# Kernel tuning notes

Hardware: AMD Instinct MI355X
Metric: run time of the kernel (lower is better)

Reference implementation:

```python
import jax, jax.numpy as jnp
import numpy as np

B, C, H, W = 32, 256, 7, 7
HEADS = 8
DIM_HEAD = 64
INNER = HEADS * DIM_HEAD  # 512
N_ANGLES = 16
KS = 5
GROUPS = 32
EPS = 1e-5


def setup_inputs() -> dict:
    key = jax.random.key(0)
    ks = jax.random.split(key, 16)
    w = lambda k, shp: jax.random.normal(k, shp, jnp.float32) * 0.05
    return {
        'x': jax.random.normal(ks[0], (B, C, H, W), jnp.float32),
        'gn_g': jnp.ones((C,), jnp.float32), 'gn_b': jnp.zeros((C,), jnp.float32),
        'sa_w1': w(ks[1], (C // 8, C)), 'sa_b1': jnp.zeros((C // 8,), jnp.float32),
        'sa_w2': w(ks[2], (C, C // 8)), 'sa_b2': jnp.zeros((C,), jnp.float32),
        'sa_gn_g': jnp.ones((C,), jnp.float32), 'sa_gn_b': jnp.zeros((C,), jnp.float32),
        'ra_gn_g': jnp.ones((C,), jnp.float32), 'ra_gn_b': jnp.zeros((C,), jnp.float32),
        'ra_qkv_w': w(ks[3], (3 * C, C)),
        'ra_proj_w': w(ks[4], (C, C)), 'ra_proj_b': jnp.zeros((C,), jnp.float32),
        'aa_ln_g': jnp.ones((C,), jnp.float32), 'aa_ln_b': jnp.zeros((C,), jnp.float32),
        'aa_qkv_w': w(ks[5], (3 * INNER, C)),
        'aa_relpos': w(ks[6], (2 * 7 - 1, 2 * 7 - 1, HEADS)),
        'aa_out_w': w(ks[7], (C, INNER)), 'aa_out_b': jnp.zeros((C,), jnp.float32),
        'ad_dir_w': w(ks[8], (N_ANGLES, C, C, KS, KS)),
        'ad_ap_w1': w(ks[9], (128, C)), 'ad_ap_b1': jnp.zeros((128,), jnp.float32),
        'ad_ap_w2': w(ks[10], (N_ANGLES, 128)), 'ad_ap_b2': jnp.zeros((N_ANGLES,), jnp.float32),
        'ad_proj_w': w(ks[11], (C, C)), 'ad_proj_b': jnp.zeros((C,), jnp.float32),
        'gate_w': w(ks[12], (4, C)), 'gate_b': jnp.zeros((4,), jnp.float32),
        'proj_w': w(ks[13], (C, C)), 'proj_b': jnp.zeros((C,), jnp.float32),
    }


def _gn(x, g, b):
    Bx, Cx, Hx, Wx = x.shape
    xr = x.reshape(Bx, GROUPS, -1)
    m = xr.mean(-1, keepdims=True)
    v = xr.var(-1, keepdims=True)
    xn = ((xr - m) * jax.lax.rsqrt(v + EPS)).reshape(Bx, Cx, Hx, Wx)
    return xn * g[None, :, None, None] + b[None, :, None, None]


def _c1(x, w, b=None):
    y = jnp.einsum('bchw,oc->bohw', x, w)
    return y if b is None else y + b[None, :, None, None]


def _rot_attn_pass(x, qkv_w):
    Bx, Cx, Hx, Wx = x.shape
    d = Cx // HEADS
    q, k, v = jnp.split(_c1(x, qkv_w), 3, axis=1)
    sh = lambda t: t.reshape(Bx, HEADS, d, Hx * Wx).transpose(0, 1, 3, 2)  # b h n d
    q, k, v = sh(q), sh(k), sh(v)
    a = jax.nn.softmax(jnp.einsum('bhid,bhjd->bhij', q, k) * (d ** -0.5), axis=-1)
    o = jnp.einsum('bhij,bhjd->bhid', a, v)
    return o.transpose(0, 1, 3, 2).reshape(Bx, Cx, Hx, Wx)


def _forward(x, gn_g, gn_b, sa_w1, sa_b1, sa_w2, sa_b2, sa_gn_g, sa_gn_b,
             ra_gn_g, ra_gn_b, ra_qkv_w, ra_proj_w, ra_proj_b,
             aa_ln_g, aa_ln_b, aa_qkv_w, aa_relpos, aa_out_w, aa_out_b,
             ad_dir_w, ad_ap_w1, ad_ap_b1, ad_ap_w2, ad_ap_b2, ad_proj_w, ad_proj_b,
             gate_w, gate_b, proj_w, proj_b):
    normed = _gn(x, gn_g, gn_b)

    # --- SpatialAttention branch ---
    wts = jax.nn.sigmoid(_c1(jax.nn.relu(_c1(normed, sa_w1, sa_b1)), sa_w2, sa_b2))
    spatial = _gn(normed * wts + normed, sa_gn_g, sa_gn_b)

    # --- RotationAwareAttention branch: 4 rot90 passes, max-fused ---
    xr = _gn(normed, ra_gn_g, ra_gn_b)
    r0 = _rot_attn_pass(xr, ra_qkv_w)
    r1 = jnp.rot90(_rot_attn_pass(jnp.rot90(xr, 1, (2, 3)), ra_qkv_w), 3, (2, 3))
    r2 = jnp.rot90(_rot_attn_pass(jnp.rot90(xr, 2, (2, 3)), ra_qkv_w), 2, (2, 3))
    r3 = jnp.rot90(_rot_attn_pass(jnp.rot90(xr, 3, (2, 3)), ra_qkv_w), 1, (2, 3))
    mx = jnp.maximum(jnp.maximum(r0, r1), jnp.maximum(r2, r3))
    rotation = _c1(mx, ra_proj_w, ra_proj_b) + normed

    # --- AngleAwareSelfAttention branch (rel-pos-biased MHSA over 49 tokens) ---
    Nn = H * W
    t = normed.reshape(B, C, Nn).transpose(0, 2, 1)  # [B,N,C]
    mu = t.mean(-1, keepdims=True)
    var = t.var(-1, keepdims=True)
    tn = (t - mu) * jax.lax.rsqrt(var + EPS) * aa_ln_g + aa_ln_b
    q, k, v = jnp.split(jnp.einsum('bnc,oc->bno', tn, aa_qkv_w), 3, axis=-1)
    sh = lambda u: u.reshape(B, Nn, HEADS, DIM_HEAD).transpose(0, 2, 1, 3)
    q, k, v = sh(q), sh(k), sh(v)
    dots = jnp.einsum('bhid,bhjd->bhij', q, k) * (DIM_HEAD ** -0.5)
    idx = jnp.arange(Nn)
    yi, xi = idx // W, idx % W
    dy = yi[None, :] - yi[:, None] + (H - 1)  # offsets into 13x13 table
    dx = xi[None, :] - xi[:, None] + (W - 1)
    bias = aa_relpos[dy, dx].transpose(2, 0, 1)[None]  # [1,heads,N,N]
    attn = jax.nn.softmax(dots + bias, axis=-1)
    o = jnp.einsum('bhij,bhjd->bhid', attn, v).transpose(0, 2, 1, 3).reshape(B, Nn, INNER)
    o = jnp.einsum('bni,oi->bno', o, aa_out_w) + aa_out_b
    angle = o.transpose(0, 2, 1).reshape(B, C, H, W) + normed

    # --- AngleAdaptiveAttention branch: 16 directional 5x5 convs + learned softmax gate ---
    dir_out = jax.lax.conv_general_dilated(
        normed, ad_dir_w.reshape(N_ANGLES * C, C, KS, KS), (1, 1), 'SAME',
        dimension_numbers=('NCHW', 'OIHW', 'NCHW')).reshape(B, N_ANGLES, C, H, W)
    gap = normed.mean((2, 3))  # [B,C]
    h1 = jax.nn.relu(gap @ ad_ap_w1.T + ad_ap_b1)
    aw = jax.nn.softmax(h1 @ ad_ap_w2.T + ad_ap_b2, axis=1)  # [B,16]
    comb = jnp.einsum('bkchw,bk->bchw', dir_out, aw)
    adaptive = _c1(comb, ad_proj_w, ad_proj_b) + normed

    # --- gated fusion ---
    gates = jax.nn.softmax(_c1(x, gate_w, gate_b), axis=1)  # [B,4,H,W]
    fused = (spatial * gates[:, 0:1] + rotation * gates[:, 1:2]
             + angle * gates[:, 2:3] + adaptive * gates[:, 3:4])
    return _c1(fused, proj_w, proj_b) + x


def reference(x, gn_g, gn_b, sa_w1, sa_b1, sa_w2, sa_b2, sa_gn_g, sa_gn_b,
              ra_gn_g, ra_gn_b, ra_qkv_w, ra_proj_w, ra_proj_b,
              aa_ln_g, aa_ln_b, aa_qkv_w, aa_relpos, aa_out_w, aa_out_b,
              ad_dir_w, ad_ap_w1, ad_ap_b1, ad_ap_w2, ad_ap_b2, ad_proj_w, ad_proj_b,
              gate_w, gate_b, proj_w, proj_b):
    return _forward(x, gn_g, gn_b, sa_w1, sa_b1, sa_w2, sa_b2, sa_gn_g, sa_gn_b,
                    ra_gn_g, ra_gn_b, ra_qkv_w, ra_proj_w, ra_proj_b,
                    aa_ln_g, aa_ln_b, aa_qkv_w, aa_relpos, aa_out_w, aa_out_b,
                    ad_dir_w, ad_ap_w1, ad_ap_b1, ad_ap_w2, ad_ap_b2, ad_proj_w, ad_proj_b,
                    gate_w, gate_b, proj_w, proj_b)
```

## Files before the change

kernel.cpp:

```cpp
#include <hip/hip_runtime.h>

#define EPS 1e-5f
typedef unsigned short u16;
typedef unsigned int u32;
typedef float f32x4 __attribute__((ext_vector_type(4)));
typedef short bf16x8 __attribute__((ext_vector_type(8)));

__device__ __forceinline__ float bf2f(u16 h){
  return __uint_as_float(((u32)h) << 16);
}
__device__ __forceinline__ u16 f2bf(float f){
  u32 u = __float_as_uint(f);
  u += 0x7fffu + ((u >> 16) & 1u);
  return (u16)(u >> 16);
}
__device__ __forceinline__ u32 pk2(float lo, float hi){
  return ((u32)f2bf(hi) << 16) | (u32)f2bf(lo);
}
union BF8 { bf16x8 v; u32 u[4]; };

__global__ __launch_bounds__(256) void k_prep1(
    const float* __restrict__ x, const float* __restrict__ gn_g, const float* __restrict__ gn_b,
    const float* __restrict__ ra_g, const float* __restrict__ ra_b,
    float* __restrict__ normed, float* __restrict__ xr, float* __restrict__ gap)
{
  int ch = blockIdx.x, b = blockIdx.y;
  int c0 = ch * 32;
  __shared__ float xs[1568], ns[1568];
  const float* xb = x + ((size_t)b * 256 + c0) * 49;
  for (int i = threadIdx.x; i < 1568; i += 256) xs[i] = xb[i];
  __syncthreads();
  int wv = threadIdx.x >> 6, lane = threadIdx.x & 63;
  const float* gsrc = xs + wv * 392;
  float* ndst = ns + wv * 392;
  float s = 0.f, ss = 0.f;
  for (int i = lane; i < 392; i += 64){ float v = gsrc[i]; s += v; ss += v * v; }
  for (int off = 32; off; off >>= 1){ s += __shfl_down(s, off); ss += __shfl_down(ss, off); }
  s = __shfl(s, 0); ss = __shfl(ss, 0);
  float m = s / 392.f, rs = rsqrtf(ss / 392.f - m * m + EPS);
  for (int i = lane; i < 392; i += 64){
    int c = c0 + wv * 8 + i / 49;
    ndst[i] = (gsrc[i] - m) * rs * gn_g[c] + gn_b[c];
  }
  __syncthreads();
  float* nb = normed + ((size_t)b * 256 + c0) * 49;
  for (int i = threadIdx.x; i < 1568; i += 256) nb[i] = ns[i];
  if (threadIdx.x < 32){
    float g2 = 0.f; const float* rp = ns + threadIdx.x * 49;
    for (int p = 0; p < 49; p++) g2 += rp[p];
    gap[(size_t)b * 256 + c0 + threadIdx.x] = g2 * (1.f / 49.f);
  }
  s = 0.f; ss = 0.f;
  for (int i = lane; i < 392; i += 64){ float v = ndst[i]; s += v; ss += v * v; }
  for (int off = 32; off; off >>= 1){ s += __shfl_down(s, off); ss += __shfl_down(ss, off); }
  s = __shfl(s, 0); ss = __shfl(ss, 0);
  m = s / 392.f; rs = rsqrtf(ss / 392.f - m * m + EPS);
  float* xrb = xr + ((size_t)b * 256 + c0) * 49;
  for (int i = lane; i < 392; i += 64){
    int c = c0 + wv * 8 + i / 49;
    xrb[wv * 392 + i] = (ndst[i] - m) * rs * ra_g[c] + ra_b[c];
  }
}

__global__ __launch_bounds__(256) void k_pos(
    const float* __restrict__ x, const float* __restrict__ normed,
    const float* __restrict__ gate_w, const float* __restrict__ gate_b,
    float* __restrict__ gates_g, float* __restrict__ lnm_g, float* __restrict__ lnr_g)
{
  int pc = blockIdx.x, b = blockIdx.y;
  __shared__ float gw[1024];
  for (int i = threadIdx.x; i < 1024; i += 256) gw[i] = gate_w[i];
  __syncthreads();
  int wv = threadIdx.x >> 6, lane = threadIdx.x & 63;
  for (int pi = wv; pi < 7; pi += 4){
    int p = pc * 7 + pi;
    const float* nb = normed + (size_t)b * 12544 + p;
    const float* xb = x + (size_t)b * 12544 + p;
    float s = 0.f, ss = 0.f, g0 = 0.f, g1 = 0.f, g2 = 0.f, g3 = 0.f;
    for (int c = lane; c < 256; c += 64){
      float nv = nb[c * 49];
      float xv = xb[c * 49];
      s += nv; ss += nv * nv;
      g0 += xv * gw[c]; g1 += xv * gw[256 + c];
      g2 += xv * gw[512 + c]; g3 += xv * gw[768 + c];
    }
    for (int off = 32; off; off >>= 1){
      s += __shfl_down(s, off); ss += __shfl_down(ss, off);
      g0 += __shfl_down(g0, off); g1 += __shfl_down(g1, off);
      g2 += __shfl_down(g2, off); g3 += __shfl_down(g3, off);
    }
    if (lane == 0){
      float mu = s / 256.f;
      lnm_g[b * 49 + p] = mu;
      lnr_g[b * 49 + p] = rsqrtf(ss / 256.f - mu * mu + EPS);
      g0 += gate_b[0]; g1 += gate_b[1]; g2 += gate_b[2]; g3 += gate_b[3];
      float mx = fmaxf(fmaxf(g0, g1), fmaxf(g2, g3));
      float e0 = __expf(g0 - mx), e1 = __expf(g1 - mx), e2 = __expf(g2 - mx), e3 = __expf(g3 - mx);
      float inv = 1.f / (e0 + e1 + e2 + e3);
      float* gg = gates_g + (size_t)b * 196 + p;
      gg[0] = e0 * inv; gg[49] = e1 * inv; gg[98] = e2 * inv; gg[147] = e3 * inv;
    }
  }
}

__global__ __launch_bounds__(256) void k_h1aw(
    const float* __restrict__ normed, const float* __restrict__ sa_w1, const float* __restrict__ sa_b1,
    const float* __restrict__ ap_w1, const float* __restrict__ ap_b1,
    const float* __restrict__ ap_w2, const float* __restrict__ ap_b2,
    const float* __restrict__ gap_g,
    float* __restrict__ h1_g, float* __restrict__ aw_g)
{
  int xb2 = blockIdx.x, b = blockIdx.y;
  int t = threadIdx.x;
  if (xb2 == 7){
    __shared__ float gaps[256], h[128], lg[16];
    gaps[t] = gap_g[b * 256 + t];
    __syncthreads();
    if (t < 128){
      float s = ap_b1[t];
      const float* wr = ap_w1 + t * 256;
      #pragma unroll 4
      for (int c = 0; c < 256; c++) s += gaps[c] * wr[c];
      h[t] = fmaxf(s, 0.f);
    }
    __syncthreads();
    if (t < 16){
      float s = ap_b2[t];
      const float* wr = ap_w2 + t * 128;
      #pragma unroll 4
      for (int o = 0; o < 128; o++) s += h[o] * wr[o];
      lg[t] = s;
    }
    __syncthreads();
    if (t == 0){
      float mx = -1e30f;
      for (int k = 0; k < 16; k++) mx = fmaxf(mx, lg[k]);
      float e[16], sm = 0.f;
      for (int k = 0; k < 16; k++){ e[k] = __expf(lg[k] - mx); sm += e[k]; }
      float inv = 1.f / sm;
      for (int k = 0; k < 16; k++) aw_g[b * 16 + k] = e[k] * inv;
    }
    return;
  }
  __shared__ float w1t[256 * 33];
  __shared__ float ns2[256 * 7];
  int p0 = xb2 * 7;
  for (int i = t; i < 8192; i += 256){
    int o = i >> 8, c = i & 255;
    w1t[c * 33 + o] = sa_w1[i];
  }
  for (int i = t; i < 1792; i += 256){
    int c = i / 7, pl = i - c * 7;
    ns2[i] = normed[(size_t)b * 12544 + c * 49 + p0 + pl];
  }
  __syncthreads();
  if (t < 224){
    int pl = t >> 5, o = t & 31;
    float s = sa_b1[o];
    #pragma unroll 8
    for (int c = 0; c < 256; c++) s += ns2[c * 7 + pl] * w1t[c * 33 + o];
    h1_g[(size_t)b * 1568 + (p0 + pl) * 32 + o] = fmaxf(s, 0.f);
  }
}

__global__ __launch_bounds__(256) void k_spatial(
    const float* __restrict__ normed, const float* __restrict__ h1_g,
    const float* __restrict__ sa_w2, const float* __restrict__ sa_b2,
    const float* __restrict__ sa_g, const float* __restrict__ sa_bb,
    float* __restrict__ spat_g)
{
  int gc = blockIdx.x, b = blockIdx.y;
  __shared__ float h1s[49 * 33];
  __shared__ float w2s[1024];
  int t = threadIdx.x;
  for (int i = t; i < 1568; i += 256){
    int p = i >> 5, o = i & 31;
    h1s[p * 33 + o] = h1_g[(size_t)b * 1568 + i];
  }
  for (int i = t; i < 1024; i += 256) w2s[i] = sa_w2[gc * 1024 + i];
  __syncthreads();
  int wv = t >> 6, lane = t & 63;
  int cg0 = wv * 8;
  const float* nb = normed + (size_t)b * 12544 + (gc * 32 + cg0) * 49;
  float tmp[7];
  float s = 0.f, ss = 0.f;
  #pragma unroll
  for (int j = 0; j < 7; j++){
    int i = lane + 64 * j;
    float v = 0.f;
    if (i < 392){
      int c = i / 49;
      const float* wr = w2s + (cg0 + c) * 32;
      const float* hp = h1s + (i - c * 49) * 33;
      float d = sa_b2[gc * 32 + cg0 + c];
      #pragma unroll
      for (int o = 0; o < 32; o++) d += hp[o] * wr[o];
      v = nb[i] * (1.f + 1.f / (1.f + __expf(-d)));
      s += v; ss += v * v;
    }
    tmp[j] = v;
  }
  for (int off = 32; off; off >>= 1){ s += __shfl_down(s, off); ss += __shfl_down(ss, off); }
  s = __shfl(s, 0); ss = __shfl(ss, 0);
  float m = s / 392.f, rs = rsqrtf(ss / 392.f - m * m + EPS);
  float* sb = spat_g + (size_t)b * 12544 + (gc * 32 + cg0) * 49;
  #pragma unroll
  for (int j = 0; j < 7; j++){
    int i = lane + 64 * j;
    if (i < 392){
      int c = gc * 32 + cg0 + i / 49;
      sb[i] = (tmp[j] - m) * rs * sa_g[c] + sa_bb[c];
    }
  }
}

__global__ __launch_bounds__(256) void k_weff(
    const float* __restrict__ W, const float* __restrict__ aw, u16* __restrict__ weff)
{
  __shared__ float aws[512];
  for (int i = threadIdx.x; i < 512; i += 256) aws[i] = aw[i];
  size_t j = (size_t)blockIdx.x * 1024 + (size_t)threadIdx.x * 4;
  float4 wv[16];
  #pragma unroll
  for (int k = 0; k < 16; k++)
    wv[k] = *(const float4*)(W + (size_t)k * 1638400 + j);
  __syncthreads();
  #pragma unroll 1
  for (int b = 0; b < 32; b++){
    const float* a = aws + b * 16;
    float a0 = 0.f, a1 = 0.f, a2 = 0.f, a3 = 0.f;
    #pragma unroll
    for (int k = 0; k < 16; k++){
      float s = a[k];
      a0 += s * wv[k].x; a1 += s * wv[k].y; a2 += s * wv[k].z; a3 += s * wv[k].w;
    }
    ushort4 o;
    o.x = f2bf(a0); o.y = f2bf(a1); o.z = f2bf(a2); o.w = f2bf(a3);
    *(ushort4*)(weff + (size_t)b * 1638400 + j) = o;
  }
}

__global__ __launch_bounds__(256) void k_conv(
    const u16* __restrict__ weff, const float* __restrict__ normed, float* __restrict__ comb_part)
{
  int part = blockIdx.x, b = blockIdx.y;
  int co = threadIdx.x;
  __shared__ float xs[784];
  const float* nb = normed + ((size_t)b * 256 + part * 16) * 49;
  for (int i = co; i < 784; i += 256) xs[i] = nb[i];
  __syncthreads();
  float acc[49];
  #pragma unroll
  for (int p = 0; p < 49; p++) acc[p] = 0.f;
  const u16* wr = weff + (size_t)b * 1638400 + (size_t)co * 6400 + part * 400;
  #pragma unroll 1
  for (int ci = 0; ci < 16; ci++){
    float ximg[49];
    #pragma unroll
    for (int p = 0; p < 49; p++) ximg[p] = xs[ci * 49 + p];
    float wv[25];
    #pragma unroll
    for (int s2 = 0; s2 < 25; s2++) wv[s2] = bf2f(wr[ci * 25 + s2]);
    #pragma unroll
    for (int sy = 0; sy < 5; sy++){
      #pragma unroll
      for (int sx = 0; sx < 5; sx++){
        float w = wv[sy * 5 + sx];
        #pragma unroll
        for (int py = 0; py < 7; py++){
          int iy = py + sy - 2;
          if (iy < 0 || iy >= 7) continue;
          #pragma unroll
          for (int px = 0; px < 7; px++){
            int ix = px + sx - 2;
            if (ix < 0 || ix >= 7) continue;
            acc[py * 7 + px] += w * ximg[iy * 7 + ix];
          }
        }
      }
    }
  }
  float* op = comb_part + (((size_t)part * 32 + b) * 256 + co) * 49;
  #pragma unroll
  for (int p = 0; p < 49; p++) op[p] = acc[p];
}

__global__ __launch_bounds__(256) void k_comb_reduce(
    const float* __restrict__ part, float* __restrict__ comb)
{
  int i = blockIdx.x * 256 + threadIdx.x;
  if (i >= 100352) return;
  float a0 = 0.f, a1 = 0.f, a2 = 0.f, a3 = 0.f;
  #pragma unroll
  for (int p = 0; p < 16; p++){
    float4 v = ((const float4*)part)[(size_t)p * 100352 + i];
    a0 += v.x; a1 += v.y; a2 += v.z; a3 += v.w;
  }
  float4 o; o.x = a0; o.y = a1; o.z = a2; o.w = a3;
  ((float4*)comb)[i] = o;
}

__device__ __forceinline__ void mfma_gemm_dev(
    const float* __restrict__ W, const float* __restrict__ bias,
    const float* __restrict__ act, const float* __restrict__ res,
    float* __restrict__ out, int M, int K, int m0blk, int p0, int b,
    const float* __restrict__ lnm, const float* __restrict__ lnr,
    const float* __restrict__ lng, const float* __restrict__ lnb)
{
  int wv = threadIdx.x >> 6, lane = threadIdx.x & 63;
  int lo = lane & 15, hi = lane >> 4;
  int m0 = m0blk + wv * 32;
  int p = p0 + lo;
  bool pok = p < 49;
  const float* ab = act + (size_t)b * K * 49;
  float lm = 0.f, lr = 0.f;
  if (lng && pok){ lm = lnm[p]; lr = lnr[p]; }
  f32x4 acc0 = {0.f, 0.f, 0.f, 0.f};
  f32x4 acc1 = {0.f, 0.f, 0.f, 0.f};
  const float* wr0 = W + (size_t)(m0 + lo) * K + hi * 8;
  const float* wr1 = W + (size_t)(m0 + 16 + lo) * K + hi * 8;
  for (int k0 = 0; k0 < K; k0 += 32){
    int kb = k0 + hi * 8;
    float4 a0lo = *(const float4*)(wr0 + k0);
    float4 a0hi = *(const float4*)(wr0 + k0 + 4);
    float4 a1lo = *(const float4*)(wr1 + k0);
    float4 a1hi = *(const float4*)(wr1 + k0 + 4);
    float bv[8];
    if (pok){
      const float* ap = ab + (size_t)kb * 49 + p;
      #pragma unroll
      for (int i = 0; i < 8; i++) bv[i] = ap[i * 49];
      if (lng){
        #pragma unroll
        for (int i = 0; i < 8; i++) bv[i] = (bv[i] - lm) * lr * lng[kb + i] + lnb[kb + i];
      }
    } else {
      #pragma unroll
      for (int i = 0; i < 8; i++) bv[i] = 0.f;
    }
    BF8 A0, A1, B;
    A0.u[0] = pk2(a0lo.x, a0lo.y); A0.u[1] = pk2(a0lo.z, a0lo.w);
    A0.u[2] = pk2(a0hi.x, a0hi.y); A0.u[3] = pk2(a0hi.z, a0hi.w);
    A1.u[0] = pk2(a1lo.x, a1lo.y); A1.u[1] = pk2(a1lo.z, a1lo.w);
    A1.u[2] = pk2(a1hi.x, a1hi.y); A1.u[3] = pk2(a1hi.z, a1hi.w);
    B.u[0] = pk2(bv[0], bv[1]); B.u[1] = pk2(bv[2], bv[3]);
    B.u[2] = pk2(bv[4], bv[5]); B.u[3] = pk2(bv[6], bv[7]);
    acc0 = __builtin_amdgcn_mfma_f32_16x16x32_bf16(A0.v, B.v, acc0, 0, 0, 0);
    acc1 = __builtin_amdgcn_mfma_f32_16x16x32_bf16(A1.v, B.v, acc1, 0, 0, 0);
  }
  if (pok){
    #pragma unroll
    for (int r = 0; r < 4; r++){
      int m = m0 + hi * 4 + r;
      size_t idx = ((size_t)b * M + m) * 49 + p;
      float v = acc0[r] + (bias ? bias[m] : 0.f);
      if (res) v += res[idx];
      out[idx] = v;
      int m2 = m + 16;
      size_t idx2 = idx + 16 * 49;
      float v2 = acc1[r] + (bias ? bias[m2] : 0.f);
      if (res) v2 += res[idx2];
      out[idx2] = v2;
    }
  }
}

__global__ __launch_bounds__(256) void k_qkv(
    const float* __restrict__ ra_w, const float* __restrict__ aa_w,
    const float* __restrict__ xr, const float* __restrict__ normed,
    const float* __restrict__ lnm, const float* __restrict__ lnr,
    const float* __restrict__ ln_g, const float* __restrict__ ln_b,
    float* __restrict__ ra_qkv, float* __restrict__ aa_qkv)
{
  int bx = blockIdx.x, b = blockIdx.y;
  if (bx < 24){
    int m0 = (bx >> 2) * 128, p0 = (bx & 3) * 16;
    mfma_gemm_dev(ra_w, nullptr, xr, nullptr, ra_qkv, 768, 256, m0, p0, b,
                  nullptr, nullptr, nullptr, nullptr);
  } else {
    int bx2 = bx - 24;
    int m0 = (bx2 >> 2) * 128, p0 = (bx2 & 3) * 16;
    mfma_gemm_dev(aa_w, nullptr, normed, nullptr, aa_qkv, 1536, 256, m0, p0, b,
                  lnm + b * 49, lnr + b * 49, ln_g, ln_b);
  }
}

__global__ __launch_bounds__(256) void k_proj3(
    const float* __restrict__ ra_pw, const float* __restrict__ ra_pb, const float* __restrict__ r0,
    const float* __restrict__ aa_ow, const float* __restrict__ aa_ob, const float* __restrict__ aa_o,
    const float* __restrict__ ad_pw, const float* __restrict__ ad_pb, const float* __restrict__ comb,
    const float* __restrict__ normed,
    float* __restrict__ rotf, float* __restrict__ angf, float* __restrict__ adpf)
{
  int bx = blockIdx.x, b = blockIdx.y;
  if (bx < 8){
    int m0 = (bx >> 2) * 128, p0 = (bx & 3) * 16;
    mfma_gemm_dev(ra_pw, ra_pb, r0, normed, rotf, 256, 256, m0, p0, b,
                  nullptr, nullptr, nullptr, nullptr);
  } else if (bx < 16){
    int bx2 = bx - 8;
    int m0 = (bx2 >> 2) * 128, p0 = (bx2 & 3) * 16;
    mfma_gemm_dev(aa_ow, aa_ob, aa_o, normed, angf, 256, 512, m0, p0, b,
                  nullptr, nullptr, nullptr, nullptr);
  } else {
    int bx2 = bx - 16;
    int m0 = (bx2 >> 2) * 128, p0 = (bx2 & 3) * 16;
    mfma_gemm_dev(ad_pw, ad_pb, comb, normed, adpf, 256, 256, m0, p0, b,
                  nullptr, nullptr, nullptr, nullptr);
  }
}

__global__ __launch_bounds__(256) void k_fusion(
    const float* __restrict__ spat, const float* __restrict__ rotf,
    const float* __restrict__ angf, const float* __restrict__ adpf,
    const float* __restrict__ gates, float* __restrict__ fused)
{
  int i = blockIdx.x * 256 + threadIdx.x;
  int b = i / 12544, r = i - b * 12544;
  int p = r % 49;
  const float* g = gates + (size_t)b * 196;
  fused[i] = spat[i] * g[p] + rotf[i] * g[49 + p] + angf[i] * g[98 + p] + adpf[i] * g[147 + p];
}

__global__ __launch_bounds__(256) void k_final(
    const float* __restrict__ proj_w, const float* __restrict__ proj_b,
    const float* __restrict__ fused, const float* __restrict__ x,
    float* __restrict__ out)
{
  int bx = blockIdx.x, b = blockIdx.y;
  int m0 = (bx >> 2) * 128, p0 = (bx & 3) * 16;
  mfma_gemm_dev(proj_w, proj_b, fused, x, out, 256, 256, m0, p0, b,
                nullptr, nullptr, nullptr, nullptr);
}

__global__ __launch_bounds__(256) void k_attn(
    const float* __restrict__ ra_qkv, const float* __restrict__ aa_qkv,
    const float* __restrict__ relpos,
    float* __restrict__ r0, float* __restrict__ ao)
{
  __shared__ float sm[3 * 49 * 65 + 49 * 52];
  int xb2 = blockIdx.x, b = blockIdx.y;
  if (xb2 < 8){
    int hd = xb2;
    float* qs = sm; float* ks = sm + 1617; float* vs = sm + 3234; float* sc = sm + 4851;
    const float* base = ra_qkv + (size_t)b * 768 * 49;
    for (int i = threadIdx.x; i < 1568; i += 256){
      int d = i / 49, tok = i - d * 49;
      qs[tok * 33 + d] = base[(hd * 32 + d) * 49 + tok];
      ks[tok * 33 + d] = base[(256 + hd * 32 + d) * 49 + tok];
      vs[tok * 33 + d] = base[(512 + hd * 32 + d) * 49 + tok];
    }
    __syncthreads();
    const float scale = 0.17677669529663687f;
    for (int it = threadIdx.x; it < 2401; it += 256){
      int i = it / 49, j = it - i * 49;
      float s = 0.f;
      #pragma unroll
      for (int d = 0; d < 32; d++) s += qs[i * 33 + d] * ks[j * 33 + d];
      sc[i * 52 + j] = s * scale;
    }
    __syncthreads();
    if (threadIdx.x < 49){
      int i = threadIdx.x;
      float mx = -1e30f;
      for (int j = 0; j < 49; j++) mx = fmaxf(mx, sc[i * 52 + j]);
      float smm = 0.f;
      for (int j = 0; j < 49; j++){ float e = __expf(sc[i * 52 + j] - mx); sc[i * 52 + j] = e; smm += e; }
      float inv = 1.f / smm;
      for (int j = 0; j < 49; j++) sc[i * 52 + j] *= inv;
    }
    __syncthreads();
    for (int it = threadIdx.x; it < 1568; it += 256){
      int d = it / 49, i = it - d * 49;
      float o = 0.f;
      for (int j = 0; j < 49; j++) o += sc[i * 52 + j] * vs[j * 33 + d];
      r0[((size_t)b * 256 + hd * 32 + d) * 49 + i] = o;
    }
  } else {
    int hd = xb2 - 8;
    float* qs = sm; float* ks = sm + 3185; float* vs = sm + 6370; float* sc = sm + 9555;
    const float* base = aa_qkv + (size_t)b * 1536 * 49;
    for (int i = threadIdx.x; i < 3136; i += 256){
      int d = i / 49, tok = i - d * 49;
      qs[tok * 65 + d] = base[(hd * 64 + d) * 49 + tok];
      ks[tok * 65 + d] = base[(512 + hd * 64 + d) * 49 + tok];
      vs[tok * 65 + d] = base[(1024 + hd * 64 + d) * 49 + tok];
    }
    __syncthreads();
    for (int it = threadIdx.x; it < 2401; it += 256){
      int i = it / 49, j = it - i * 49;
      float s = 0.f;
      #pragma unroll
      for (int d = 0; d < 64; d++) s += qs[i * 65 + d] * ks[j * 65 + d];
      int dy = j / 7 - i / 7 + 6, dx = j % 7 - i % 7 + 6;
      sc[i * 52 + j] = s * 0.125f + relpos[(dy * 13 + dx) * 8 + hd];
    }
    __syncthreads();
    if (threadIdx.x < 49){
      int i = threadIdx.x;
      float mx = -1e30f;
      for (int j = 0; j < 49; j++) mx = fmaxf(mx, sc[i * 52 + j]);
      float smm = 0.f;
      for (int j = 0; j < 49; j++){ float e = __expf(sc[i * 52 + j] - mx); sc[i * 52 + j] = e; smm += e; }
      float inv = 1.f / smm;
      for (int j = 0; j < 49; j++) sc[i * 52 + j] *= inv;
    }
    __syncthreads();
    for (int it = threadIdx.x; it < 3136; it += 256){
      int d = it / 49, i = it - d * 49;
      float o = 0.f;
      for (int j = 0; j < 49; j++) o += sc[i * 52 + j] * vs[j * 65 + d];
      ao[((size_t)b * 512 + hd * 64 + d) * 49 + i] = o;
    }
  }
}

extern "C" void kernel_launch(void* const* d_in, const int* in_sizes, int n_in,
                              void* d_out, int out_size, void* d_ws, size_t ws_size,
                              hipStream_t stream)
{
  const float* x        = (const float*)d_in[0];
  const float* gn_g     = (const float*)d_in[1];
  const float* gn_b     = (const float*)d_in[2];
  const float* sa_w1    = (const float*)d_in[3];
  const float* sa_b1    = (const float*)d_in[4];
  const float* sa_w2    = (const float*)d_in[5];
  const float* sa_b2    = (const float*)d_in[6];
  const float* sa_gn_g  = (const float*)d_in[7];
  const float* sa_gn_b  = (const float*)d_in[8];
  const float* ra_gn_g  = (const float*)d_in[9];
  const float* ra_gn_b  = (const float*)d_in[10];
  const float* ra_qkv_w = (const float*)d_in[11];
  const float* ra_proj_w= (const float*)d_in[12];
  const float* ra_proj_b= (const float*)d_in[13];
  const float* aa_ln_g  = (const float*)d_in[14];
  const float* aa_ln_b  = (const float*)d_in[15];
  const float* aa_qkv_w = (const float*)d_in[16];
  const float* aa_relpos= (const float*)d_in[17];
  const float* aa_out_w = (const float*)d_in[18];
  const float* aa_out_b = (const float*)d_in[19];
  const float* ad_dir_w = (const float*)d_in[20];
  const float* ad_ap_w1 = (const float*)d_in[21];
  const float* ad_ap_b1 = (const float*)d_in[22];
  const float* ad_ap_w2 = (const float*)d_in[23];
  const float* ad_ap_b2 = (const float*)d_in[24];
  const float* ad_proj_w= (const float*)d_in[25];
  const float* ad_proj_b= (const float*)d_in[26];
  const float* gate_w   = (const float*)d_in[27];
  const float* gate_b   = (const float*)d_in[28];
  const float* proj_w   = (const float*)d_in[29];
  const float* proj_b   = (const float*)d_in[30];

  char* ws = (char*)d_ws;
  float* normed    = (float*)(ws + 0);
  float* xr        = (float*)(ws + 1605632);
  float* h1_g      = (float*)(ws + 3211264);
  float* lnm       = (float*)(ws + 3420160);
  float* lnr       = (float*)(ws + 3426560);
  float* spatial   = (float*)(ws + 4816896);
  float* rotf      = (float*)(ws + 6422528);
  float* anglef    = (float*)(ws + 8028160);
  float* adaptf    = (float*)(ws + 9633792);
  float* fused     = (float*)(ws + 11239424);
  float* r0        = (float*)(ws + 12845056);
  float* gap       = (float*)(ws + 14450688);
  float* aw        = (float*)(ws + 14483456);
  float* gates     = (float*)(ws + 14485504);
  float* ra_qkv    = (float*)(ws + 14510592);
  float* aa_qkv    = (float*)(ws + 19327488);
  float* aa_o      = (float*)(ws + 28961280);
  float* comb      = (float*)(ws + 32172544);
  float* comb_part = (float*)(ws + 33778176);
  u16*   weff      = (u16*)  (ws + 59468288);

  float* out = (float*)d_out;

  k_prep1<<<dim3(8, 32), 256, 0, stream>>>(x, gn_g, gn_b, ra_gn_g, ra_gn_b, normed, xr, gap);
  k_pos<<<dim3(7, 32), 256, 0, stream>>>(x, normed, gate_w, gate_b, gates, lnm, lnr);
  k_h1aw<<<dim3(8, 32), 256, 0, stream>>>(normed, sa_w1, sa_b1,
                                          ad_ap_w1, ad_ap_b1, ad_ap_w2, ad_ap_b2,
                                          gap, h1_g, aw);
  k_spatial<<<dim3(8, 32), 256, 0, stream>>>(normed, h1_g, sa_w2, sa_b2, sa_gn_g, sa_gn_b, spatial);
  k_weff<<<dim3(1600), 256, 0, stream>>>(ad_dir_w, aw, weff);
  k_qkv<<<dim3(72, 32), 256, 0, stream>>>(ra_qkv_w, aa_qkv_w, xr, normed,
                                          lnm, lnr, aa_ln_g, aa_ln_b, ra_qkv, aa_qkv);
  k_attn<<<dim3(16, 32), 256, 0, stream>>>(ra_qkv, aa_qkv, aa_relpos, r0, aa_o);
  k_conv<<<dim3(16, 32), 256, 0, stream>>>(weff, normed, comb_part);
  k_comb_reduce<<<dim3(392), 256, 0, stream>>>(comb_part, comb);
  k_proj3<<<dim3(24, 32), 256, 0, stream>>>(ra_proj_w, ra_proj_b, r0,
                                            aa_out_w, aa_out_b, aa_o,
                                            ad_proj_w, ad_proj_b, comb,
                                            normed, rotf, anglef, adaptf);
  k_fusion<<<dim3(1568), 256, 0, stream>>>(spatial, rotf, anglef, adaptf, gates, fused);
  k_final<<<dim3(8, 32), 256, 0, stream>>>(proj_w, proj_b, fused, x, out);
}
```

Before: 304.9 us.

## Replace scalar direct 5x5 conv with im2col plus bf16 MFMA GEMM

Adds an im2col kernel that writes the 5x5-padded patches of the normalized input as bf16 rows, one row per output pixel. The per-batch direction-weighted conv then runs as a GEMM on 16x16x32 bf16 MFMA instructions instead of scalar FP32 FMAs. The K split drops from 16 partitions to 8, so the reduction kernel sums fewer partials. In exchange it adds the im2col kernel and its buffer, pads the pixel dimension to 64 (the extra rows read neighbouring memory and are discarded), and rounds the input activations to bf16.

```diff
diff --git a/kernel.cpp b/kernel.cpp
--- a/kernel.cpp
+++ b/kernel.cpp
@@ -240,59 +240,90 @@
   }
 }
 
-__global__ __launch_bounds__(256) void k_conv(
-    const u16* __restrict__ weff, const float* __restrict__ normed, float* __restrict__ comb_part)
-{
-  int part = blockIdx.x, b = blockIdx.y;
-  int co = threadIdx.x;
-  __shared__ float xs[784];
-  const float* nb = normed + ((size_t)b * 256 + part * 16) * 49;
-  for (int i = co; i < 784; i += 256) xs[i] = nb[i];
+__global__ __launch_bounds__(256) void k_im2col(
+    const float* __restrict__ normed, u16* __restrict__ xim)
+{
+  int p = blockIdx.x, b = blockIdx.y;
+  __shared__ u16 row[6400];
+  int ci = threadIdx.x;
+  int py = p / 7, px = p - py * 7;
+  const float* nb = normed + (size_t)b * 12544 + ci * 49;
+  u16* rp = row + ci * 25;
+  #pragma unroll
+  for (int sy = 0; sy < 5; sy++){
+    int iy = py + sy - 2;
+    #pragma unroll
+    for (int sx = 0; sx < 5; sx++){
+      int ix = px + sx - 2;
+      float v = (iy >= 0 && iy < 7 && ix >= 0 && ix < 7) ? nb[iy * 7 + ix] : 0.f;
+      rp[sy * 5 + sx] = f2bf(v);
+    }
+  }
   __syncthreads();
-  float acc[49];
+  const u32* rs = (const u32*)row;
+  u32* od = (u32*)(xim + (size_t)(b * 49 + p) * 6400);
+  for (int i = threadIdx.x; i < 3200; i += 256) od[i] = rs[i];
+}
+
+__global__ __launch_bounds__(256) void k_conv_mfma(
+    const u16* __restrict__ weff, const u16* __restrict__ xim, float* __restrict__ partial)
+{
+  int bx = blockIdx.x, b = blockIdx.y;
+  int mblk = bx >> 3, kp = bx & 7;
+  int wv = threadIdx.x >> 6, lane = threadIdx.x & 63;
+  int lo = lane & 15, hi = lane >> 4;
+  int co0 = mblk * 128 + wv * 32;
+  const u16* wr0 = weff + (size_t)b * 1638400 + (size_t)(co0 + lo) * 6400 + kp * 800 + hi * 8;
+  const u16* wr1 = wr0 + 16 * 6400;
+  const u16* xb = xim + (size_t)b * 313600 + (size_t)lo * 6400 + kp * 800 + hi * 8;
+  f32x4 acc[2][4];
   #pragma unroll
-  for (int p = 0; p < 49; p++) acc[p] = 0.f;
-  const u16* wr = weff + (size_t)b * 1638400 + (size_t)co * 6400 + part * 400;
+  for (int mi = 0; mi < 2; mi++)
+    #pragma unroll
+    for (int pi = 0; pi < 4; pi++) acc[mi][pi] = (f32x4){0.f, 0.f, 0.f, 0.f};
   #pragma unroll 1
-  for (int ci = 0; ci < 16; ci++){
-    float ximg[49];
+  for (int ks = 0; ks < 25; ks++){
+    int k0 = ks * 32;
+    bf16x8 A0 = *(const bf16x8*)(wr0 + k0);
+    bf16x8 A1 = *(const bf16x8*)(wr1 + k0);
+    bf16x8 B0 = *(const bf16x8*)(xb + k0);
+    bf16x8 B1 = *(const bf16x8*)(xb + 16 * 6400 + k0);
+    bf16x8 B2 = *(const bf16x8*)(xb + 32 * 6400 + k0);
+    bf16x8 B3 = *(const bf16x8*)(xb + 48 * 6400 + k0);
+    acc[0][0] = __builtin_amdgcn_mfma_f32_16x16x32_bf16(A0, B0, acc[0][0], 0, 0, 0);
+    acc[0][1] = __builtin_amdgcn_mfma_f32_16x16x32_bf16(A0, B1, acc[0][1], 0, 0, 0);
+    acc[0][2] = __builtin_amdgcn_mfma_f32_16x16x32_bf16(A0, B2, acc[0][2], 0, 0, 0);
+    acc[0][3] = __builtin_amdgcn_mfma_f32_16x16x32_bf16(A0, B3, acc[0][3], 0, 0, 0);
+    acc[1][0] = __builtin_amdgcn_mfma_f32_16x16x32_bf16(A1, B0, acc[1][0], 0, 0, 0);
+    acc[1][1] = __builtin_amdgcn_mfma_f32_16x16x32_bf16(A1, B1, acc[1][1], 0, 0, 0);
+    acc[1][2] = __builtin_amdgcn_mfma_f32_16x16x32_bf16(A1, B2, acc[1][2], 0, 0, 0);
+    acc[1][3] = __builtin_amdgcn_mfma_f32_16x16x32_bf16(A1, B3, acc[1][3], 0, 0, 0);
+  }
+  float* pb = partial + ((size_t)kp * 32 + b) * 12544;
+  #pragma unroll
+  for (int mi = 0; mi < 2; mi++){
     #pragma unroll
-    for (int p = 0; p < 49; p++) ximg[p] = xs[ci * 49 + p];
-    float wv[25];
-    #pragma unroll
-    for (int s2 = 0; s2 < 25; s2++) wv[s2] = bf2f(wr[ci * 25 + s2]);
-    #pragma unroll
-    for (int sy = 0; sy < 5; sy++){
-      #pragma unroll
-      for (int sx = 0; sx < 5; sx++){
-        float w = wv[sy * 5 + sx];
+    for (int pi = 0; pi < 4; pi++){
+      int p = pi * 16 + lo;
+      if (p < 49){
         #pragma unroll
-        for (int py = 0; py < 7; py++){
-          int iy = py + sy - 2;
-          if (iy < 0 || iy >= 7) continue;
-          #pragma unroll
-          for (int px = 0; px < 7; px++){
-            int ix = px + sx - 2;
-            if (ix < 0 || ix >= 7) continue;
-            acc[py * 7 + px] += w * ximg[iy * 7 + ix];
-          }
+        for (int r = 0; r < 4; r++){
+          int co = co0 + mi * 16 + hi * 4 + r;
+          pb[co * 49 + p] = acc[mi][pi][r];
         }
       }
     }
   }
-  float* op = comb_part + (((size_t)part * 32 + b) * 256 + co) * 49;
-  #pragma unroll
-  for (int p = 0; p < 49; p++) op[p] = acc[p];
-}
-
-__global__ __launch_bounds__(256) void k_comb_reduce(
+}
+
+__global__ __launch_bounds__(256) void k_conv_reduce(
     const float* __restrict__ part, float* __restrict__ comb)
 {
   int i = blockIdx.x * 256 + threadIdx.x;
   if (i >= 100352) return;
   float a0 = 0.f, a1 = 0.f, a2 = 0.f, a3 = 0.f;
   #pragma unroll
-  for (int p = 0; p < 16; p++){
+  for (int p = 0; p < 8; p++){
     float4 v = ((const float4*)part)[(size_t)p * 100352 + i];
     a0 += v.x; a1 += v.y; a2 += v.z; a3 += v.w;
   }
@@ -570,8 +601,9 @@
   float* aa_qkv    = (float*)(ws + 19327488);
   float* aa_o      = (float*)(ws + 28961280);
   float* comb      = (float*)(ws + 32172544);
-  float* comb_part = (float*)(ws + 33778176);
-  u16*   weff      = (u16*)  (ws + 59468288);
+  float* partial   = (float*)(ws + 33778176);
+  u16*   xim       = (u16*)  (ws + 46623232);
+  u16*   weff      = (u16*)  (ws + 66693632);
 
   float* out = (float*)d_out;
 
@@ -582,11 +614,12 @@
                                           gap, h1_g, aw);
   k_spatial<<<dim3(8, 32), 256, 0, stream>>>(normed, h1_g, sa_w2, sa_b2, sa_gn_g, sa_gn_b, spatial);
   k_weff<<<dim3(1600), 256, 0, stream>>>(ad_dir_w, aw, weff);
+  k_im2col<<<dim3(49, 32), 256, 0, stream>>>(normed, xim);
   k_qkv<<<dim3(72, 32), 256, 0, stream>>>(ra_qkv_w, aa_qkv_w, xr, normed,
                                           lnm, lnr, aa_ln_g, aa_ln_b, ra_qkv, aa_qkv);
   k_attn<<<dim3(16, 32), 256, 0, stream>>>(ra_qkv, aa_qkv, aa_relpos, r0, aa_o);
-  k_conv<<<dim3(16, 32), 256, 0, stream>>>(weff, normed, comb_part);
-  k_comb_reduce<<<dim3(392), 256, 0, stream>>>(comb_part, comb);
+  k_conv_mfma<<<dim3(16, 32), 256, 0, stream>>>(weff, xim, partial);
+  k_conv_reduce<<<dim3(392), 256, 0, stream>>>(partial, comb);
   k_proj3<<<dim3(24, 32), 256, 0, stream>>>(ra_proj_w, ra_proj_b, r0,
                                             aa_out_w, aa_out_b, aa_o,
                                             ad_proj_w, ad_proj_b, comb,
```

After: 298.5 us. -2.1%, faster.
